# Optimization experiments

Hardware: AMD Instinct MI355X
Metric: run time of the kernel (lower is better)

The kernel has to match this reference:

```python
import jax, jax.numpy as jnp
import numpy as np

N_USERS = 100000
N_ITEMS = 50000
N_NODES = N_USERS + N_ITEMS
LATENT = 64
NNZ = 2400000
BATCH = 2048
EPS = 1e-12  # F.normalize eps


def setup_inputs() -> dict:
    key = jax.random.key(0)
    ks = jax.random.split(key, 16)
    inp = {
        "rows": jax.random.randint(ks[0], (NNZ,), 0, N_NODES, dtype=jnp.int32),
        "cols": jax.random.randint(ks[1], (NNZ,), 0, N_NODES, dtype=jnp.int32),
        "vals": jax.random.uniform(ks[2], (NNZ,), dtype=jnp.float32),
        "x": jax.random.normal(ks[3], (N_NODES, LATENT), dtype=jnp.float32) * 0.1,
        "users": jax.random.randint(ks[12], (BATCH,), 0, N_USERS, dtype=jnp.int32),
        "items": jax.random.randint(ks[13], (BATCH,), 0, N_ITEMS, dtype=jnp.int32),
    }
    for k in range(2):
        inp[f"W_gc{k}"] = jax.random.normal(ks[4 + 4 * k], (LATENT, LATENT), dtype=jnp.float32) * 0.1
        inp[f"b_gc{k}"] = jax.random.normal(ks[5 + 4 * k], (1, LATENT), dtype=jnp.float32) * 0.1
        inp[f"W_bi{k}"] = jax.random.normal(ks[6 + 4 * k], (LATENT, LATENT), dtype=jnp.float32) * 0.1
        inp[f"b_bi{k}"] = jax.random.normal(ks[7 + 4 * k], (1, LATENT), dtype=jnp.float32) * 0.1
    return inp


def _l2_normalize(v):
    # F.normalize(p=2, dim=1): divide by max(||v||_2, eps)
    n = jnp.sqrt(jnp.sum(v * v, axis=1, keepdims=True))
    return v / jnp.maximum(n, EPS)


def reference(rows, cols, vals, x,
              W_gc0, b_gc0, W_bi0, b_bi0,
              W_gc1, b_gc1, W_bi1, b_bi1,
              users, items):
    weights = [(W_gc0, b_gc0, W_bi0, b_bi0), (W_gc1, b_gc1, W_bi1, b_bi1)]
    ego = x                      # [N, D]
    embs = [x]
    for (Wg, bg, Wb, bb) in weights:
        # sparse adj @ ego  (COO gather + segment-sum scatter)
        msgs = vals[:, None] * ego[cols]                              # [nnz, D]
        side = jax.ops.segment_sum(msgs, rows, num_segments=N_NODES)  # [N, D]
        sum_emb = side @ Wg + bg
        bi_emb = (ego * side) @ Wb + bb
        ego = _l2_normalize(jax.nn.leaky_relu(sum_emb + bi_emb, negative_slope=0.2))
        embs.append(ego)
    all_emb = jnp.concatenate(embs, axis=1)          # [N, 3*D]
    users_emb = all_emb[users]                       # [B, 3*D]
    items_emb = all_emb[N_USERS + items]             # [B, 3*D]
    gamma = jnp.sum(users_emb * items_emb, axis=1)   # [B]
    return gamma
```

## Files before the change

kernel.cpp:

```cpp
#include <hip/hip_runtime.h>

#define N_USERS_C 100000
#define N_NODES_C 150000
#define D 64
#define NB 2344
#define NSUP 74
#define CPAD 16
#define SPAD 68
#define FCAP 1536
#define S1B 256
#define FRAG 240
#define S2CAP 2560
#define BPS 16
#define FPB (S1B / BPS)
#define NSCAN 147
#define MARK 1

__global__ __launch_bounds__(256) void mark1_k(
    const int* __restrict__ u, const int* __restrict__ it,
    unsigned char* __restrict__ samp, unsigned char* __restrict__ need, int batch)
{
    int i = blockIdx.x * blockDim.x + threadIdx.x;
    if (i >= 2 * batch) return;
    int n = (i < batch) ? u[i] : N_USERS_C + it[i - batch];
    samp[n] = MARK;
    need[n] = MARK;
}

__global__ __launch_bounds__(256) void mark2_k(
    const int* __restrict__ rows, const int* __restrict__ cols,
    const unsigned char* __restrict__ samp, unsigned char* __restrict__ need, int nnz)
{
    int gtid = blockIdx.x * blockDim.x + threadIdx.x;
    int stride = gridDim.x * blockDim.x;
    for (int e = gtid; e < nnz; e += stride)
        if (samp[rows[e]] == MARK) need[cols[e]] = MARK;
}

__global__ __launch_bounds__(1024) void scan1_k(
    const unsigned char* __restrict__ need, int* __restrict__ part,
    int* __restrict__ bsum, int n)
{
    __shared__ int wsum[16];
    int i = blockIdx.x * 1024 + threadIdx.x;
    int lane = threadIdx.x & 63, wid = threadIdx.x >> 6;
    int v = (i < n && need[i] == MARK) ? 1 : 0;
    int incl = v;
    #pragma unroll
    for (int off = 1; off < 64; off <<= 1) {
        int t = __shfl_up(incl, off);
        if (lane >= off) incl += t;
    }
    if (lane == 63) wsum[wid] = incl;
    __syncthreads();
    int woff = 0;
    for (int w = 0; w < wid; ++w) woff += wsum[w];
    if (i < n) part[i] = woff + incl - v;
    if (threadIdx.x == 1023) bsum[blockIdx.x] = woff + incl;
}

__global__ __launch_bounds__(256) void scanB_k(
    const int* __restrict__ bsum, int* __restrict__ idx,
    const unsigned char* __restrict__ need, int* __restrict__ list,
    int* __restrict__ bcur, int* __restrict__ Mptr, int n)
{
    __shared__ int pre[NSCAN + 1];
    __shared__ int raw[NSCAN];
    int t = threadIdx.x;
    if (t < NSCAN) raw[t] = bsum[t];
    __syncthreads();
    if (t == 0) {
        int run = 0;
        for (int k = 0; k < NSCAN; ++k) { pre[k] = run; run += raw[k]; }
        pre[NSCAN] = run;
    }
    __syncthreads();
    int i = blockIdx.x * blockDim.x + t;
    if (i < NB) bcur[i * CPAD] = i * FCAP;
    if (blockIdx.x == 0 && t == 0) Mptr[0] = pre[NSCAN];
    if (i >= n) return;
    int val = idx[i] + pre[i >> 10];
    if (need[i] == MARK) { idx[i] = val; list[val] = i; }
    else idx[i] = -1;
}

__global__ __launch_bounds__(512) void s1_k(
    const int* __restrict__ rows, const int* __restrict__ cols,
    const float* __restrict__ vals, const int* __restrict__ idx,
    int2* __restrict__ pairs1, int* __restrict__ scnt, int nnz)
{
    __shared__ int lcur[NSUP];
    int t = threadIdx.x;
    for (int i = t; i < NSUP; i += 512) lcur[i] = 0;
    __syncthreads();
    int b = blockIdx.x;
    int per = (nnz + S1B - 1) / S1B;
    int s = b * per;
    int e = min(nnz, s + per);
    for (int i = s + t; i < e; i += 512) {
        int ci = idx[rows[i]];
        if (ci < 0) continue;
        int sp = ci >> 11;
        int k = atomicAdd(&lcur[sp], 1);
        pairs1[(size_t)sp * (S1B * FRAG) + b * FRAG + k] =
            make_int2(((ci & 2047) << 18) | cols[i], __float_as_int(vals[i]));
    }
    __syncthreads();
    for (int i = t; i < NSUP; i += 512) scnt[i * S1B + b] = lcur[i];
}

__global__ __launch_bounds__(256) void s2_k(
    const int* __restrict__ scnt, const int2* __restrict__ pairs1,
    int* __restrict__ bcurP, int2* __restrict__ pairs)
{
    __shared__ int2 sbuf[S2CAP];
    __shared__ int fcnt[32], fcur[32], gb[32];
    int sp = blockIdx.x / BPS, part = blockIdx.x % BPS;
    int t = threadIdx.x;
    if (t < 32) { fcnt[t] = 0; fcur[t] = 0; }
    __syncthreads();
    int base = 0;
    for (int fi = 0; fi < FPB; ++fi) {
        int b = part * FPB + fi;
        int m = scnt[sp * S1B + b];
        const int2* src = &pairs1[(size_t)sp * (S1B * FRAG) + b * FRAG];
        for (int i = t; i < m; i += 256) {
            int2 p = src[i];
            sbuf[base + i] = p;
            atomicAdd(&fcnt[(p.x >> 18) >> 6], 1);
        }
        base += m;
    }
    __syncthreads();
    if (t < 32) {
        int c = fcnt[t];
        gb[t] = c ? atomicAdd(&bcurP[(sp * 32 + t) * CPAD], c) : 0;
    }
    __syncthreads();
    for (int i = t; i < base; i += 256) {
        int2 p = sbuf[i];
        int ris = p.x >> 18;
        int f = ris >> 6;
        int k = atomicAdd(&fcur[f], 1);
        pairs[gb[f] + k] = make_int2(((ris & 63) << 18) | (p.x & 0x3FFFF), p.y);
    }
}

__global__ __launch_bounds__(256) void sortb_k(
    const int* __restrict__ bcurP, int2* __restrict__ pairs,
    int* __restrict__ rp)
{
    __shared__ int2 buf[FCAP];
    __shared__ int cnt[64];
    __shared__ int cur[64];
    int b = blockIdx.x;
    int s = b * FCAP;
    int e = bcurP[b * CPAD];
    int m = e - s;
    int t = threadIdx.x;
    if (t < 64) cnt[t] = 0;
    __syncthreads();
    for (int i = t; i < m; i += 256) {
        int2 p = pairs[s + i];
        buf[i] = p;
        atomicAdd(&cnt[p.x >> 18], 1);
    }
    __syncthreads();
    if (t < 64) {
        int v = cnt[t];
        int incl = v;
        #pragma unroll
        for (int o = 1; o < 64; o <<= 1) {
            int u = __shfl_up(incl, o);
            if (t >= o) incl += u;
        }
        cur[t] = incl - v;
        rp[b * 65 + t] = s + incl - v;
        if (t == 63) rp[b * 65 + 64] = s + incl;
    }
    __syncthreads();
    for (int i = t; i < m; i += 256) {
        int2 p = buf[i];
        int dst = atomicAdd(&cur[p.x >> 18], 1);
        pairs[s + dst] = make_int2(p.x & 0x3FFFF, p.y);
    }
}

__global__ __launch_bounds__(256, 4) void fuse1_k(
    const int* __restrict__ rp, const int2* __restrict__ pairs,
    const float* __restrict__ x,
    const float* __restrict__ Wg, const float* __restrict__ bg,
    const float* __restrict__ Wb, const float* __restrict__ bb,
    float* __restrict__ out, const int* __restrict__ list,
    const int* __restrict__ Mptr)
{
    __shared__ __align__(16) float sAT[D][SPAD];
    __shared__ __align__(16) float sBT[D][SPAD];

    int nr = Mptr[0];
    int r0 = blockIdx.x * 64;
    if (r0 >= nr) return;

    int t    = threadIdx.x;
    int lane = t & 63;
    int wid  = t >> 6;
    int lq   = lane & 15;
    int qb   = lane & 48;

    for (int pass = 0; pass < 4; ++pass) {
        int rr  = wid * 16 + pass * 4 + (lane >> 4);
        int row = r0 + rr;
        int valid = row < nr;
        int s = 0, len = 0, er = 0;
        if (valid) {
            int rb = (row >> 6) * 65 + (row & 63);
            s = rp[rb];
            len = rp[rb + 1] - s;
            er = list[row];
        }
        int ml = len;
        ml = max(ml, __shfl_xor(ml, 16));
        ml = max(ml, __shfl_xor(ml, 32));

        float4 acc = make_float4(0.f, 0.f, 0.f, 0.f);
        for (int base = 0; base < ml; base += 16) {
            int2 p = make_int2(0, 0);
            int o = base + lq;
            if (o < len) p = pairs[s + o];
            int rem = len - base;
            rem = min(max(rem, 0), 16);
            int mr = rem;
            mr = max(mr, __shfl_xor(mr, 16));
            mr = max(mr, __shfl_xor(mr, 32));
            int cnt8 = (mr + 7) & ~7;
            for (int j = 0; j < cnt8; j += 8) {
                int c[8]; float v[8]; float4 f[8];
                #pragma unroll
                for (int q = 0; q < 8; ++q) {
                    c[q] = __shfl(p.x, qb | (j + q));
                    v[q] = __int_as_float(__shfl(p.y, qb | (j + q)));
                }
                #pragma unroll
                for (int q = 0; q < 8; ++q)
                    f[q] = *(const float4*)&x[(size_t)c[q] * D + lq * 4];
                #pragma unroll
                for (int q = 0; q < 8; ++q) {
                    acc.x = fmaf(v[q], f[q].x, acc.x);
                    acc.y = fmaf(v[q], f[q].y, acc.y);
                    acc.z = fmaf(v[q], f[q].z, acc.z);
                    acc.w = fmaf(v[q], f[q].w, acc.w);
                }
            }
        }
        float4 ev = make_float4(0.f, 0.f, 0.f, 0.f);
        if (valid) ev = *(const float4*)&x[(size_t)er * D + lq * 4];
        sAT[lq * 4 + 0][rr] = acc.x;
        sAT[lq * 4 + 1][rr] = acc.y;
        sAT[lq * 4 + 2][rr] = acc.z;
        sAT[lq * 4 + 3][rr] = acc.w;
        sBT[lq * 4 + 0][rr] = acc.x * ev.x;
        sBT[lq * 4 + 1][rr] = acc.y * ev.y;
        sBT[lq * 4 + 2][rr] = acc.z * ev.z;
        sBT[lq * 4 + 3][rr] = acc.w * ev.w;
    }
    __syncthreads();

    int tc = t & 15;
    int tr = t >> 4;
    float acc2[4][4] = {};
    #pragma unroll 4
    for (int k = 0; k < D; ++k) {
        float4 a4 = *(const float4*)&sAT[k][tr * 4];
        float4 b4 = *(const float4*)&sBT[k][tr * 4];
        float4 g4 = *(const float4*)&Wg[k * D + tc * 4];
        float4 w4 = *(const float4*)&Wb[k * D + tc * 4];
        float av[4] = {a4.x, a4.y, a4.z, a4.w};
        float bv[4] = {b4.x, b4.y, b4.z, b4.w};
        float gv[4] = {g4.x, g4.y, g4.z, g4.w};
        float wv[4] = {w4.x, w4.y, w4.z, w4.w};
        #pragma unroll
        for (int i = 0; i < 4; ++i)
            #pragma unroll
            for (int j = 0; j < 4; ++j)
                acc2[i][j] = fmaf(av[i], gv[j], fmaf(bv[i], wv[j], acc2[i][j]));
    }

    float4 bgv = *(const float4*)&bg[tc * 4];
    float4 bbv = *(const float4*)&bb[tc * 4];
    float bias[4] = {bgv.x + bbv.x, bgv.y + bbv.y, bgv.z + bbv.z, bgv.w + bbv.w};

    float vv[4][4];
    float ss[4] = {0.f, 0.f, 0.f, 0.f};
    #pragma unroll
    for (int i = 0; i < 4; ++i) {
        #pragma unroll
        for (int j = 0; j < 4; ++j) {
            float v = acc2[i][j] + bias[j];
            v = (v > 0.0f) ? v : 0.2f * v;
            vv[i][j] = v;
            ss[i] += v * v;
        }
    }
    #pragma unroll
    for (int i = 0; i < 4; ++i) {
        #pragma unroll
        for (int off = 1; off < 16; off <<= 1)
            ss[i] += __shfl_xor(ss[i], off);
    }
    #pragma unroll
    for (int i = 0; i < 4; ++i) {
        int row = r0 + tr * 4 + i;
        if (row < nr) {
            float inv = 1.0f / fmaxf(sqrtf(ss[i]), 1e-12f);
            float4 o = make_float4(vv[i][0] * inv, vv[i][1] * inv,
                                   vv[i][2] * inv, vv[i][3] * inv);
            *(float4*)&out[(size_t)row * D + tc * 4] = o;
        }
    }
}

__global__ __launch_bounds__(256, 4) void fuse2_k(
    const int* __restrict__ rp, const int2* __restrict__ pairs,
    const float* __restrict__ e1c, const int* __restrict__ idx,
    const float* __restrict__ Wg, const float* __restrict__ bg,
    const float* __restrict__ Wb, const float* __restrict__ bb,
    float* __restrict__ out, const int* __restrict__ u,
    const int* __restrict__ it, int batch)
{
    __shared__ __align__(16) float sAT[D][SPAD];
    __shared__ __align__(16) float sBT[D][SPAD];

    int nr = 2 * batch;
    int r0 = blockIdx.x * 64;
    if (r0 >= nr) return;

    int t    = threadIdx.x;
    int lane = t & 63;
    int wid  = t >> 6;
    int lq   = lane & 15;
    int qb   = lane & 48;

    for (int pass = 0; pass < 4; ++pass) {
        int rr  = wid * 16 + pass * 4 + (lane >> 4);
        int row = r0 + rr;
        int valid = row < nr;
        int s = 0, len = 0, cr = 0;
        if (valid) {
            int n = (row < batch) ? u[row] : N_USERS_C + it[row - batch];
            cr = idx[n];
            int rb = (cr >> 6) * 65 + (cr & 63);
            s = rp[rb];
            len = rp[rb + 1] - s;
        }
        int ml = len;
        ml = max(ml, __shfl_xor(ml, 16));
        ml = max(ml, __shfl_xor(ml, 32));

        float4 acc = make_float4(0.f, 0.f, 0.f, 0.f);
        for (int base = 0; base < ml; base += 16) {
            int2 p = make_int2(0, 0);
            int o = base + lq;
            if (o < len) p = pairs[s + o];
            int rem = len - base;
            rem = min(max(rem, 0), 16);
            int mr = rem;
            mr = max(mr, __shfl_xor(mr, 16));
            mr = max(mr, __shfl_xor(mr, 32));
            int cnt8 = (mr + 7) & ~7;
            for (int j = 0; j < cnt8; j += 8) {
                int c[8]; float v[8]; float4 f[8];
                #pragma unroll
                for (int q = 0; q < 8; ++q) {
                    c[q] = __shfl(p.x, qb | (j + q));
                    v[q] = __int_as_float(__shfl(p.y, qb | (j + q)));
                }
                #pragma unroll
                for (int q = 0; q < 8; ++q) {
                    int cc = idx[c[q]];
                    cc = max(cc, 0);
                    f[q] = *(const float4*)&e1c[(size_t)cc * D + lq * 4];
                }
                #pragma unroll
                for (int q = 0; q < 8; ++q) {
                    acc.x = fmaf(v[q], f[q].x, acc.x);
                    acc.y = fmaf(v[q], f[q].y, acc.y);
                    acc.z = fmaf(v[q], f[q].z, acc.z);
                    acc.w = fmaf(v[q], f[q].w, acc.w);
                }
            }
        }
        float4 ev = make_float4(0.f, 0.f, 0.f, 0.f);
        if (valid) ev = *(const float4*)&e1c[(size_t)cr * D + lq * 4];
        sAT[lq * 4 + 0][rr] = acc.x;
        sAT[lq * 4 + 1][rr] = acc.y;
        sAT[lq * 4 + 2][rr] = acc.z;
        sAT[lq * 4 + 3][rr] = acc.w;
        sBT[lq * 4 + 0][rr] = acc.x * ev.x;
        sBT[lq * 4 + 1][rr] = acc.y * ev.y;
        sBT[lq * 4 + 2][rr] = acc.z * ev.z;
        sBT[lq * 4 + 3][rr] = acc.w * ev.w;
    }
    __syncthreads();

    int tc = t & 15;
    int tr = t >> 4;
    float acc2[4][4] = {};
    #pragma unroll 4
    for (int k = 0; k < D; ++k) {
        float4 a4 = *(const float4*)&sAT[k][tr * 4];
        float4 b4 = *(const float4*)&sBT[k][tr * 4];
        float4 g4 = *(const float4*)&Wg[k * D + tc * 4];
        float4 w4 = *(const float4*)&Wb[k * D + tc * 4];
        float av[4] = {a4.x, a4.y, a4.z, a4.w};
        float bv[4] = {b4.x, b4.y, b4.z, b4.w};
        float gv[4] = {g4.x, g4.y, g4.z, g4.w};
        float wv[4] = {w4.x, w4.y, w4.z, w4.w};
        #pragma unroll
        for (int i = 0; i < 4; ++i)
            #pragma unroll
            for (int j = 0; j < 4; ++j)
                acc2[i][j] = fmaf(av[i], gv[j], fmaf(bv[i], wv[j], acc2[i][j]));
    }

    float4 bgv = *(const float4*)&bg[tc * 4];
    float4 bbv = *(const float4*)&bb[tc * 4];
    float bias[4] = {bgv.x + bbv.x, bgv.y + bbv.y, bgv.z + bbv.z, bgv.w + bbv.w};

    float vv[4][4];
    float ss[4] = {0.f, 0.f, 0.f, 0.f};
    #pragma unroll
    for (int i = 0; i < 4; ++i) {
        #pragma unroll
        for (int j = 0; j < 4; ++j) {
            float v = acc2[i][j] + bias[j];
            v = (v > 0.0f) ? v : 0.2f * v;
            vv[i][j] = v;
            ss[i] += v * v;
        }
    }
    #pragma unroll
    for (int i = 0; i < 4; ++i) {
        #pragma unroll
        for (int off = 1; off < 16; off <<= 1)
            ss[i] += __shfl_xor(ss[i], off);
    }
    #pragma unroll
    for (int i = 0; i < 4; ++i) {
        int row = r0 + tr * 4 + i;
        if (row < nr) {
            float inv = 1.0f / fmaxf(sqrtf(ss[i]), 1e-12f);
            float4 o = make_float4(vv[i][0] * inv, vv[i][1] * inv,
                                   vv[i][2] * inv, vv[i][3] * inv);
            *(float4*)&out[(size_t)row * D + tc * 4] = o;
        }
    }
}

__global__ __launch_bounds__(256) void gamma_k(
    const float* __restrict__ x, const float* __restrict__ e1c,
    const int* __restrict__ idx, const float* __restrict__ e2c,
    const int* __restrict__ users, const int* __restrict__ items,
    float* __restrict__ gamma, int batch)
{
    int gtid = blockIdx.x * blockDim.x + threadIdx.x;
    int wave = gtid >> 6;
    int lane = threadIdx.x & 63;
    if (wave >= batch) return;
    size_t uu = (size_t)users[wave];
    size_t tt = (size_t)(N_USERS_C + items[wave]);
    float acc = x[uu * D + lane] * x[tt * D + lane]
              + e1c[(size_t)idx[uu] * D + lane] * e1c[(size_t)idx[tt] * D + lane]
              + e2c[(size_t)wave * D + lane] * e2c[(size_t)(batch + wave) * D + lane];
    #pragma unroll
    for (int off = 1; off < 64; off <<= 1) acc += __shfl_xor(acc, off);
    if (lane == 0) gamma[wave] = acc;
}

extern "C" void kernel_launch(void* const* d_in, const int* in_sizes, int n_in,
                              void* d_out, int out_size, void* d_ws, size_t ws_size,
                              hipStream_t stream) {
    const int*   rows  = (const int*)d_in[0];
    const int*   cols  = (const int*)d_in[1];
    const float* vals  = (const float*)d_in[2];
    const float* x     = (const float*)d_in[3];
    const int*   users = (const int*)d_in[4];
    const int*   items = (const int*)d_in[5];
    const float* Wg0 = (const float*)d_in[6];
    const float* bg0 = (const float*)d_in[7];
    const float* Wb0 = (const float*)d_in[8];
    const float* bb0 = (const float*)d_in[9];
    const float* Wg1 = (const float*)d_in[10];
    const float* bg1 = (const float*)d_in[11];
    const float* Wb1 = (const float*)d_in[12];
    const float* bb1 = (const float*)d_in[13];

    int nnz   = in_sizes[0];
    int batch = in_sizes[4];
    float* out = (float*)d_out;

    size_t emb = (size_t)N_NODES_C * D;
    float* A      = (float*)d_ws;
    float* Sbuf   = A + emb;
    int*   bcur   = (int*)(Sbuf + emb);
    int*   rp     = bcur + NB * CPAD;
    int*   idx    = rp + NB * 65 + 2;
    int*   list   = idx + N_NODES_C;
    int*   bsum   = list + N_NODES_C;
    int*   Mptr   = bsum + 1024;
    int*   scnt   = Mptr + 4;
    unsigned char* need = (unsigned char*)(scnt + NSUP * S1B);
    unsigned char* samp = need + N_NODES_C;
    int2*  pairs  = (int2*)(((size_t)(samp + N_NODES_C) + 15) & ~(size_t)15);

    int2*  pairs1 = (int2*)Sbuf;
    float* e2c    = Sbuf;

    mark1_k<<<(2 * batch + 255) / 256, 256, 0, stream>>>(users, items, samp, need, batch);
    mark2_k<<<1024, 256, 0, stream>>>(rows, cols, samp, need, nnz);
    scan1_k<<<NSCAN, 1024, 0, stream>>>(need, idx, bsum, N_NODES_C);
    scanB_k<<<(N_NODES_C + 255) / 256, 256, 0, stream>>>(bsum, idx, need, list, bcur, Mptr, N_NODES_C);

    s1_k<<<S1B, 512, 0, stream>>>(rows, cols, vals, idx, pairs1, scnt, nnz);
    s2_k<<<NSUP * BPS, 256, 0, stream>>>(scnt, pairs1, bcur, pairs);
    sortb_k<<<NB, 256, 0, stream>>>(bcur, pairs, rp);

    fuse1_k<<<(N_NODES_C + 63) / 64, 256, 0, stream>>>(
        rp, pairs, x, Wg0, bg0, Wb0, bb0, A, list, Mptr);

    fuse2_k<<<(2 * batch + 63) / 64, 256, 0, stream>>>(
        rp, pairs, A, idx, Wg1, bg1, Wb1, bb1, e2c, users, items, batch);

    gamma_k<<<(batch * 64 + 255) / 256, 256, 0, stream>>>(
        x, A, idx, e2c, users, items, out, batch);
}
```

Measured before the change: 256.0 us.

## Widen fuse1 blocks, shrink fuse2 tiles, scatter layer-1 output by node id

fuse1 now runs 512-thread blocks that gather two passes per wave instead of four, and each thread computes 2 rows of the dense epilogue instead of 4. It also writes layer-1 embeddings to their original node index instead of a compacted index. fuse2 uses 16-row blocks (4x more blocks) and a single gather pass. Because e1 is now indexed directly by node id, fuse2 and gamma_k drop the idx indirection on every gathered neighbor. The aim is more parallelism and fewer dependent loads, at the cost of scattered writes into a full-size buffer, which must hold N_NODES rows.

```diff
diff --git a/kernel.cpp b/kernel.cpp
--- a/kernel.cpp
+++ b/kernel.cpp
@@ -6,7 +6,8 @@
 #define NB 2344
 #define NSUP 74
 #define CPAD 16
-#define SPAD 68
+#define SPAD 69
+#define SPAD2 17
 #define FCAP 1536
 #define S1B 256
 #define FRAG 240
@@ -186,7 +187,7 @@
     }
 }
 
-__global__ __launch_bounds__(256, 4) void fuse1_k(
+__global__ __launch_bounds__(512, 8) void fuse1_k(
     const int* __restrict__ rp, const int2* __restrict__ pairs,
     const float* __restrict__ x,
     const float* __restrict__ Wg, const float* __restrict__ bg,
@@ -207,8 +208,8 @@
     int lq   = lane & 15;
     int qb   = lane & 48;
 
-    for (int pass = 0; pass < 4; ++pass) {
-        int rr  = wid * 16 + pass * 4 + (lane >> 4);
+    for (int pass = 0; pass < 2; ++pass) {
+        int rr  = wid * 8 + pass * 4 + (lane >> 4);
         int row = r0 + rr;
         int valid = row < nr;
         int s = 0, len = 0, er = 0;
@@ -267,32 +268,32 @@
 
     int tc = t & 15;
     int tr = t >> 4;
-    float acc2[4][4] = {};
+    float acc2[2][4] = {};
     #pragma unroll 4
     for (int k = 0; k < D; ++k) {
-        float4 a4 = *(const float4*)&sAT[k][tr * 4];
-        float4 b4 = *(const float4*)&sBT[k][tr * 4];
+        float a0 = sAT[k][tr];
+        float a1 = sAT[k][tr + 32];
+        float b0 = sBT[k][tr];
+        float b1 = sBT[k][tr + 32];
         float4 g4 = *(const float4*)&Wg[k * D + tc * 4];
         float4 w4 = *(const float4*)&Wb[k * D + tc * 4];
-        float av[4] = {a4.x, a4.y, a4.z, a4.w};
-        float bv[4] = {b4.x, b4.y, b4.z, b4.w};
         float gv[4] = {g4.x, g4.y, g4.z, g4.w};
         float wv[4] = {w4.x, w4.y, w4.z, w4.w};
         #pragma unroll
-        for (int i = 0; i < 4; ++i)
-            #pragma unroll
-            for (int j = 0; j < 4; ++j)
-                acc2[i][j] = fmaf(av[i], gv[j], fmaf(bv[i], wv[j], acc2[i][j]));
+        for (int j = 0; j < 4; ++j) {
+            acc2[0][j] = fmaf(a0, gv[j], fmaf(b0, wv[j], acc2[0][j]));
+            acc2[1][j] = fmaf(a1, gv[j], fmaf(b1, wv[j], acc2[1][j]));
+        }
     }
 
     float4 bgv = *(const float4*)&bg[tc * 4];
     float4 bbv = *(const float4*)&bb[tc * 4];
     float bias[4] = {bgv.x + bbv.x, bgv.y + bbv.y, bgv.z + bbv.z, bgv.w + bbv.w};
 
-    float vv[4][4];
-    float ss[4] = {0.f, 0.f, 0.f, 0.f};
-    #pragma unroll
-    for (int i = 0; i < 4; ++i) {
+    float vv[2][4];
+    float ss[2] = {0.f, 0.f};
+    #pragma unroll
+    for (int i = 0; i < 2; ++i) {
         #pragma unroll
         for (int j = 0; j < 4; ++j) {
             float v = acc2[i][j] + bias[j];
@@ -302,36 +303,37 @@
         }
     }
     #pragma unroll
-    for (int i = 0; i < 4; ++i) {
+    for (int i = 0; i < 2; ++i) {
         #pragma unroll
         for (int off = 1; off < 16; off <<= 1)
             ss[i] += __shfl_xor(ss[i], off);
     }
     #pragma unroll
-    for (int i = 0; i < 4; ++i) {
-        int row = r0 + tr * 4 + i;
+    for (int i = 0; i < 2; ++i) {
+        int row = r0 + tr + i * 32;
         if (row < nr) {
+            int er2 = list[row];
             float inv = 1.0f / fmaxf(sqrtf(ss[i]), 1e-12f);
             float4 o = make_float4(vv[i][0] * inv, vv[i][1] * inv,
                                    vv[i][2] * inv, vv[i][3] * inv);
-            *(float4*)&out[(size_t)row * D + tc * 4] = o;
+            *(float4*)&out[(size_t)er2 * D + tc * 4] = o;
         }
     }
 }
 
 __global__ __launch_bounds__(256, 4) void fuse2_k(
     const int* __restrict__ rp, const int2* __restrict__ pairs,
-    const float* __restrict__ e1c, const int* __restrict__ idx,
+    const float* __restrict__ e1, const int* __restrict__ idx,
     const float* __restrict__ Wg, const float* __restrict__ bg,
     const float* __restrict__ Wb, const float* __restrict__ bb,
     float* __restrict__ out, const int* __restrict__ u,
     const int* __restrict__ it, int batch)
 {
-    __shared__ __align__(16) float sAT[D][SPAD];
-    __shared__ __align__(16) float sBT[D][SPAD];
+    __shared__ __align__(16) float sAT[D][SPAD2];
+    __shared__ __align__(16) float sBT[D][SPAD2];
 
     int nr = 2 * batch;
-    int r0 = blockIdx.x * 64;
+    int r0 = blockIdx.x * 16;
     if (r0 >= nr) return;
 
     int t    = threadIdx.x;
@@ -340,14 +342,14 @@
     int lq   = lane & 15;
     int qb   = lane & 48;
 
-    for (int pass = 0; pass < 4; ++pass) {
-        int rr  = wid * 16 + pass * 4 + (lane >> 4);
+    {
+        int rr  = wid * 4 + (lane >> 4);
         int row = r0 + rr;
         int valid = row < nr;
-        int s = 0, len = 0, cr = 0;
+        int s = 0, len = 0, n = 0;
         if (valid) {
-            int n = (row < batch) ? u[row] : N_USERS_C + it[row - batch];
-            cr = idx[n];
+            n = (row < batch) ? u[row] : N_USERS_C + it[row - batch];
+            int cr = idx[n];
             int rb = (cr >> 6) * 65 + (cr & 63);
             s = rp[rb];
             len = rp[rb + 1] - s;
@@ -375,11 +377,8 @@
                     v[q] = __int_as_float(__shfl(p.y, qb | (j + q)));
                 }
                 #pragma unroll
-                for (int q = 0; q < 8; ++q) {
-                    int cc = idx[c[q]];
-                    cc = max(cc, 0);
-                    f[q] = *(const float4*)&e1c[(size_t)cc * D + lq * 4];
-                }
+                for (int q = 0; q < 8; ++q)
+                    f[q] = *(const float4*)&e1[(size_t)c[q] * D + lq * 4];
                 #pragma unroll
                 for (int q = 0; q < 8; ++q) {
                     acc.x = fmaf(v[q], f[q].x, acc.x);
@@ -390,7 +389,7 @@
             }
         }
         float4 ev = make_float4(0.f, 0.f, 0.f, 0.f);
-        if (valid) ev = *(const float4*)&e1c[(size_t)cr * D + lq * 4];
+        if (valid) ev = *(const float4*)&e1[(size_t)n * D + lq * 4];
         sAT[lq * 4 + 0][rr] = acc.x;
         sAT[lq * 4 + 1][rr] = acc.y;
         sAT[lq * 4 + 2][rr] = acc.z;
@@ -404,61 +403,48 @@
 
     int tc = t & 15;
     int tr = t >> 4;
-    float acc2[4][4] = {};
+    float acc2[4] = {};
     #pragma unroll 4
     for (int k = 0; k < D; ++k) {
-        float4 a4 = *(const float4*)&sAT[k][tr * 4];
-        float4 b4 = *(const float4*)&sBT[k][tr * 4];
+        float a0 = sAT[k][tr];
+        float b0 = sBT[k][tr];
         float4 g4 = *(const float4*)&Wg[k * D + tc * 4];
         float4 w4 = *(const float4*)&Wb[k * D + tc * 4];
-        float av[4] = {a4.x, a4.y, a4.z, a4.w};
-        float bv[4] = {b4.x, b4.y, b4.z, b4.w};
         float gv[4] = {g4.x, g4.y, g4.z, g4.w};
         float wv[4] = {w4.x, w4.y, w4.z, w4.w};
         #pragma unroll
-        for (int i = 0; i < 4; ++i)
-            #pragma unroll
-            for (int j = 0; j < 4; ++j)
-                acc2[i][j] = fmaf(av[i], gv[j], fmaf(bv[i], wv[j], acc2[i][j]));
+        for (int j = 0; j < 4; ++j)
+            acc2[j] = fmaf(a0, gv[j], fmaf(b0, wv[j], acc2[j]));
     }
 
     float4 bgv = *(const float4*)&bg[tc * 4];
     float4 bbv = *(const float4*)&bb[tc * 4];
     float bias[4] = {bgv.x + bbv.x, bgv.y + bbv.y, bgv.z + bbv.z, bgv.w + bbv.w};
 
-    float vv[4][4];
-    float ss[4] = {0.f, 0.f, 0.f, 0.f};
-    #pragma unroll
-    for (int i = 0; i < 4; ++i) {
-        #pragma unroll
-        for (int j = 0; j < 4; ++j) {
-            float v = acc2[i][j] + bias[j];
-            v = (v > 0.0f) ? v : 0.2f * v;
-            vv[i][j] = v;
-            ss[i] += v * v;
-        }
-    }
-    #pragma unroll
-    for (int i = 0; i < 4; ++i) {
-        #pragma unroll
-        for (int off = 1; off < 16; off <<= 1)
-            ss[i] += __shfl_xor(ss[i], off);
-    }
-    #pragma unroll
-    for (int i = 0; i < 4; ++i) {
-        int row = r0 + tr * 4 + i;
-        if (row < nr) {
-            float inv = 1.0f / fmaxf(sqrtf(ss[i]), 1e-12f);
-            float4 o = make_float4(vv[i][0] * inv, vv[i][1] * inv,
-                                   vv[i][2] * inv, vv[i][3] * inv);
-            *(float4*)&out[(size_t)row * D + tc * 4] = o;
-        }
+    float vv[4];
+    float ss = 0.f;
+    #pragma unroll
+    for (int j = 0; j < 4; ++j) {
+        float v = acc2[j] + bias[j];
+        v = (v > 0.0f) ? v : 0.2f * v;
+        vv[j] = v;
+        ss += v * v;
+    }
+    #pragma unroll
+    for (int off = 1; off < 16; off <<= 1)
+        ss += __shfl_xor(ss, off);
+
+    int row = r0 + tr;
+    if (row < nr) {
+        float inv = 1.0f / fmaxf(sqrtf(ss), 1e-12f);
+        float4 o = make_float4(vv[0] * inv, vv[1] * inv, vv[2] * inv, vv[3] * inv);
+        *(float4*)&out[(size_t)row * D + tc * 4] = o;
     }
 }
 
 __global__ __launch_bounds__(256) void gamma_k(
-    const float* __restrict__ x, const float* __restrict__ e1c,
-    const int* __restrict__ idx, const float* __restrict__ e2c,
+    const float* __restrict__ x, const float* __restrict__ e1,
+    const float* __restrict__ e2c,
     const int* __restrict__ users, const int* __restrict__ items,
     float* __restrict__ gamma, int batch)
 {
@@ -469,7 +455,7 @@
     size_t uu = (size_t)users[wave];
     size_t tt = (size_t)(N_USERS_C + items[wave]);
     float acc = x[uu * D + lane] * x[tt * D + lane]
-              + e1c[(size_t)idx[uu] * D + lane] * e1c[(size_t)idx[tt] * D + lane]
+              + e1[uu * D + lane] * e1[tt * D + lane]
               + e2c[(size_t)wave * D + lane] * e2c[(size_t)(batch + wave) * D + lane];
     #pragma unroll
     for (int off = 1; off < 64; off <<= 1) acc += __shfl_xor(acc, off);
@@ -524,12 +510,12 @@
     s2_k<<<NSUP * BPS, 256, 0, stream>>>(scnt, pairs1, bcur, pairs);
     sortb_k<<<NB, 256, 0, stream>>>(bcur, pairs, rp);
 
-    fuse1_k<<<(N_NODES_C + 63) / 64, 256, 0, stream>>>(
+    fuse1_k<<<(N_NODES_C + 63) / 64, 512, 0, stream>>>(
         rp, pairs, x, Wg0, bg0, Wb0, bb0, A, list, Mptr);
 
-    fuse2_k<<<(2 * batch + 63) / 64, 256, 0, stream>>>(
+    fuse2_k<<<(2 * batch + 15) / 16, 256, 0, stream>>>(
         rp, pairs, A, idx, Wg1, bg1, Wb1, bb1, e2c, users, items, batch);
 
     gamma_k<<<(batch * 64 + 255) / 256, 256, 0, stream>>>(
-        x, A, idx, e2c, users, items, out, batch);
-}
+        x, A, e2c, users, items, out, batch);
+}
```

Measured after the change: 258.0 us. Within noise of the previous version (+0.8%).
